# Optimization experiments

Hardware: AMD Instinct MI355X
Metric: run time of the kernel (lower is better)

The kernel has to match this reference:

```python
import jax, jax.numpy as jnp
import numpy as np
from jax import lax

W_BCE, W_DICE, W_FT, W_HD = 1.0, 1.0, 1.0, 0.1
TV_ALPHA, TV_BETA, TV_GAMMA = 0.7, 0.3, 0.75
HD_MAX_DIST, HD_BK = 10, 3
SMOOTH, EPS, HD_EPS = 1e-6, 1e-7, 1e-8


def _max_pool(x, k):
    # torch F.max_pool2d pads with -inf implicitly
    pad = k // 2
    return lax.reduce_window(x, -jnp.inf, lax.max, (1, 1, k, k), (1, 1, 1, 1),
                             [(0, 0), (0, 0), (pad, pad), (pad, pad)])


def _min_pool(x, k):
    pad = k // 2
    return lax.reduce_window(x, jnp.inf, lax.min, (1, 1, k, k), (1, 1, 1, 1),
                             [(0, 0), (0, 0), (pad, pad), (pad, pad)])


def _soft_boundary(mask, k):
    dil = _max_pool(mask, k)
    ero = _min_pool(mask, k)  # == -max_pool(-mask)
    return jnp.maximum(dil - ero, 0.0)


def _bce_with_logits(logits, target):
    # numerically stable: max(x,0) - x*t + log1p(exp(-|x|))
    return jnp.mean(jnp.maximum(logits, 0.0) - logits * target +
                    jnp.log1p(jnp.exp(-jnp.abs(logits))))


def _dice_loss(probs, target):
    p = probs.reshape(probs.shape[0], -1)
    t = target.reshape(target.shape[0], -1)
    inter = jnp.sum(p * t, axis=1)
    denom = jnp.sum(p, axis=1) + jnp.sum(t, axis=1)
    dice = (2.0 * inter + SMOOTH) / (denom + SMOOTH + EPS)
    return jnp.mean(1.0 - dice)


def _focal_tversky(probs, target):
    p = probs.reshape(probs.shape[0], -1)
    t = target.reshape(target.shape[0], -1)
    TP = jnp.sum(p * t, axis=1)
    FP = jnp.sum(p * (1.0 - t), axis=1)
    FN = jnp.sum((1.0 - p) * t, axis=1)
    tv = (TP + SMOOTH) / (TP + TV_ALPHA * FP + TV_BETA * FN + SMOOTH + EPS)
    return jnp.mean(jnp.power(1.0 - tv, TV_GAMMA))


def _hausdorff_surrogate(probs, target):
    pred_b = _soft_boundary(probs, HD_BK)
    gt_b = _soft_boundary(target, HD_BK)
    total = jnp.zeros((), probs.dtype)
    weight_sum = 0.0
    for d in range(1, HD_MAX_DIST + 1):
        pred_d = _max_pool(pred_b, 2 * d + 1)
        gt_d = _max_pool(gt_b, 2 * d + 1)
        w = float(d) / float(HD_MAX_DIST)
        total = total + w * (jnp.mean(jnp.abs(pred_d - gt_b)) +
                             jnp.mean(jnp.abs(gt_d - pred_b)))
        weight_sum += w
    return total / (weight_sum + HD_EPS)


def setup_inputs() -> dict:
    key = jax.random.key(0)
    k1, k2 = jax.random.split(key)
    B, C, H, W = 16, 1, 512, 512
    logits = jax.random.normal(k1, (B, C, H, W), dtype=jnp.float32)
    target = jax.random.randint(k2, (B, C, H, W), 0, 2, dtype=jnp.int32)
    return {"logits": logits, "target": target}


def reference(logits, target):
    t = target.astype(jnp.float32)
    bce = _bce_with_logits(logits, t)
    probs = jax.nn.sigmoid(logits)
    d = _dice_loss(probs, t)
    ft = _focal_tversky(probs, t)
    hd = _hausdorff_surrogate(probs, t)
    return W_BCE * bce + W_DICE * d + W_FT * ft + W_HD * hd
```

## Files before the change

kernel.cpp:

```cpp
#include <hip/hip_runtime.h>
#include <math.h>

namespace {

constexpr int B = 16, H = 512, W = 512;
constexpr int HWc = H * W;
constexpr size_t Nc = (size_t)B * HWc;

constexpr int NSTRIP = 13;
constexpr int CENT = 42;
constexpr int NBAND = 16;
constexpr int NWORK = NSTRIP * NBAND * B * 2;
constexpr int NSB = NWORK / 4;
constexpr int NBCE = B * 64;


template <int CTRL>
__device__ __forceinline__ float dpp_shift1(float v) {
  int i = __float_as_int(v);
  int r = __builtin_amdgcn_update_dpp(i, i, CTRL, 0xF, 0xF, false);
  return __int_as_float(r);
}
template <int CTRL>
__device__ __forceinline__ unsigned dpp_shift1u(unsigned v) {
  return (unsigned)__builtin_amdgcn_update_dpp((int)v, (int)v, CTRL, 0xF, 0xF,
                                               false);
}

__device__ __forceinline__ float hmax3(float v) {
  return fmaxf(fmaxf(dpp_shift1<0x138>(v), v), dpp_shift1<0x130>(v));
}
__device__ __forceinline__ void hminmax3(float v, float& mx, float& mn) {
  float s1 = dpp_shift1<0x138>(v);
  float s2 = dpp_shift1<0x130>(v);
  mx = fmaxf(fmaxf(s1, v), s2);
  mn = fminf(fminf(s1, v), s2);
}

__device__ __forceinline__ unsigned long long or3_lanes(unsigned long long v) {
  unsigned lo = (unsigned)v, hi = (unsigned)(v >> 32);
  unsigned rlo = dpp_shift1u<0x138>(lo) | lo | dpp_shift1u<0x130>(lo);
  unsigned rhi = dpp_shift1u<0x138>(hi) | hi | dpp_shift1u<0x130>(hi);
  return ((unsigned long long)rhi << 32) | rlo;
}
__device__ __forceinline__ unsigned long long and3_lanes(unsigned long long v) {
  unsigned lo = (unsigned)v, hi = (unsigned)(v >> 32);
  unsigned rlo = dpp_shift1u<0x138>(lo) & lo & dpp_shift1u<0x130>(lo);
  unsigned rhi = dpp_shift1u<0x138>(hi) & hi & dpp_shift1u<0x130>(hi);
  return ((unsigned long long)rhi << 32) | rlo;
}

__device__ __forceinline__ float wave_sum(float v) {
#pragma unroll
  for (int off = 32; off > 0; off >>= 1) v += __shfl_down(v, off);
  return v;
}

__device__ __forceinline__ float block_reduce_256(float v, float* sm, int tid) {
#pragma unroll
  for (int off = 32; off > 0; off >>= 1) v += __shfl_down(v, off);
  int lane = tid & 63, wid = tid >> 6;
  if (lane == 0) sm[wid] = v;
  __syncthreads();
  float r = 0.f;
  if (tid == 0) r = sm[0] + sm[1] + sm[2] + sm[3];
  __syncthreads();
  return r;
}

template <int CH>
__device__ __forceinline__ float load_src(const float* __restrict__ Lg,
                                          const int* __restrict__ Tg, int gy,
                                          int colc) {
  gy = min(max(gy, 0), H - 1);
  if constexpr (CH == 0) {
    float x = Lg[gy * W + colc];
    float e = __expf(-x);
    return __builtin_amdgcn_rcpf(1.f + e);
  } else {
    return (float)Tg[gy * W + colc];
  }
}

template <int D>
__device__ __forceinline__ void dilate_steps(float (&a)[52],
                                             const float (&o)[32],
                                             float (&accv)[4]) {
  if constexpr (D <= 10) {
    float hp = hmax3(a[D - 1]);
    float hc = hmax3(a[D]);
#pragma unroll
    for (int r = D; r <= 51 - D; ++r) {
      float hn = hmax3(a[r + 1]);
      float nv = fmaxf(fmaxf(hp, hc), hn);
      hp = hc;
      hc = hn;
      a[r] = nv;
    }
    constexpr float wd = 0.1f * (float)D;
#pragma unroll
    for (int k = 0; k < 32; ++k) accv[k & 3] += wd * fabsf(a[10 + k] - o[k]);
    dilate_steps<D + 1>(a, o, accv);
  }
}

__device__ __forceinline__ void fused_body0(const float* __restrict__ Lg,
                                            const int* __restrict__ Tg,
                                            int lane, int strip, int band,
                                            int bz,
                                            float* __restrict__ chain_p) {
  int col = strip * CENT - 11 + lane;
  int colc = min(max(col, 0), W - 1);
  int y0 = band * 32;

  float o[32];
  {
    float v0 = load_src<1>(Lg, Tg, y0 - 1, colc);
    float v1 = load_src<1>(Lg, Tg, y0, colc);
    float hx0, hn0, hx1, hn1;
    hminmax3(v0, hx0, hn0);
    hminmax3(v1, hx1, hn1);
#pragma unroll
    for (int k = 0; k < 32; ++k) {
      float v2 = load_src<1>(Lg, Tg, y0 + 1 + k, colc);
      float hx2, hn2;
      hminmax3(v2, hx2, hn2);
      o[k] = fmaxf(fmaxf(hx0, hx1), hx2) - fminf(fminf(hn0, hn1), hn2);
      hx0 = hx1;
      hx1 = hx2;
      hn0 = hn1;
      hn1 = hn2;
    }
  }

  float a[52];
  {
    float v0 = load_src<0>(Lg, Tg, y0 - 11, colc);
    float v1 = load_src<0>(Lg, Tg, y0 - 10, colc);
    float hx0, hn0, hx1, hn1;
    hminmax3(v0, hx0, hn0);
    hminmax3(v1, hx1, hn1);
#pragma unroll
    for (int r = 0; r < 52; ++r) {
      float v2 = load_src<0>(Lg, Tg, y0 - 9 + r, colc);
      float hx2, hn2;
      hminmax3(v2, hx2, hn2);
      a[r] = fmaxf(fmaxf(hx0, hx1), hx2) - fminf(fminf(hn0, hn1), hn2);
      hx0 = hx1;
      hx1 = hx2;
      hn0 = hn1;
      hn1 = hn2;
    }
  }

  float accv[4] = {0.f, 0.f, 0.f, 0.f};
  dilate_steps<1>(a, o, accv);
  float acc = (accv[0] + accv[1]) + (accv[2] + accv[3]);

  bool valid = (lane >= 11 && lane <= 52 && col < W);
  acc = valid ? acc : 0.f;
  acc = wave_sum(acc);
  if (lane == 0) chain_p[(bz * NBAND + band) * NSTRIP + strip] = acc;
}

__device__ __forceinline__ void fused_body1(const float* __restrict__ Lg,
                                            const int* __restrict__ Tg,
                                            int lane, int strip, int band,
                                            int bz,
                                            float* __restrict__ chain_p) {
  int col = strip * CENT - 11 + lane;
  int colc = min(max(col, 0), W - 1);
  int y0 = band * 32;

  float o[32];
  {
    float v0 = load_src<0>(Lg, Tg, y0 - 1, colc);
    float v1 = load_src<0>(Lg, Tg, y0, colc);
    float hx0, hn0, hx1, hn1;
    hminmax3(v0, hx0, hn0);
    hminmax3(v1, hx1, hn1);
#pragma unroll
    for (int k = 0; k < 32; ++k) {
      float v2 = load_src<0>(Lg, Tg, y0 + 1 + k, colc);
      float hx2, hn2;
      hminmax3(v2, hx2, hn2);
      o[k] = fmaxf(fmaxf(hx0, hx1), hx2) - fminf(fminf(hn0, hn1), hn2);
      hx0 = hx1;
      hx1 = hx2;
      hn0 = hn1;
      hn1 = hn2;
    }
  }

  unsigned long long tb = 0ull;
#pragma unroll
  for (int j = 0; j < 54; ++j) {
    int gy = min(max(y0 - 11 + j, 0), H - 1);
    tb |= (unsigned long long)(unsigned)Tg[gy * W + colc] << j;
  }

  unsigned long long vd = tb | (tb << 1) | (tb >> 1);
  unsigned long long ve = tb & (tb << 1) & (tb >> 1);
  unsigned long long ab = (or3_lanes(vd) & ~and3_lanes(ve)) >> 1;

  float accv[4] = {0.f, 0.f, 0.f, 0.f};
#pragma unroll
  for (int d = 1; d <= 10; ++d) {
    unsigned long long s = ab | (ab << 1) | (ab >> 1);
    ab = or3_lanes(s);
    const float wd = 0.1f * (float)d;
    unsigned lo = (unsigned)ab, hi = (unsigned)(ab >> 32);
#pragma unroll
    for (int k = 0; k < 32; ++k) {
      unsigned bit =
          (k < 22) ? ((lo >> (10 + k)) & 1u) : ((hi >> (k - 22)) & 1u);
      accv[k & 3] += wd * fabsf((float)bit - o[k]);
    }
  }
  float acc = (accv[0] + accv[1]) + (accv[2] + accv[3]);

  bool valid = (lane >= 11 && lane <= 52 && col < W);
  acc = valid ? acc : 0.f;
  acc = wave_sum(acc);
  if (lane == 0) chain_p[(bz * NBAND + band) * NSTRIP + strip] = acc;
}

__device__ __forceinline__ void bce_body(const float* __restrict__ logits,
                                         const int* __restrict__ target,
                                         int blk, float* __restrict__ bceA,
                                         float* __restrict__ spA,
                                         float* __restrict__ stA,
                                         float* __restrict__ sptA, float* sm) {
  int img = blk >> 6, seg = blk & 63;
  const float4* L4 =
      (const float4*)(logits + (size_t)img * HWc + (size_t)seg * 4096);
  const int4* T4 =
      (const int4*)(target + (size_t)img * HWc + (size_t)seg * 4096);
  int tid = threadIdx.x;
  float s_bce = 0.f, s_p = 0.f, s_t = 0.f, s_pt = 0.f;
#pragma unroll
  for (int it = 0; it < 4; ++it) {
    float4 x4 = L4[it * 256 + tid];
    int4 t4 = T4[it * 256 + tid];
    float xs[4] = {x4.x, x4.y, x4.z, x4.w};
    int ts[4] = {t4.x, t4.y, t4.z, t4.w};
#pragma unroll
    for (int j = 0; j < 4; ++j) {
      float x = xs[j];
      float tf = (float)ts[j];
      float e = __expf(-x);
      float p = __builtin_amdgcn_rcpf(1.f + e);
      s_p += p;
      s_t += tf;
      s_pt += p * tf;
      s_bce += x * (1.f - tf) + __logf(1.f + e);
    }
  }
  float r;
  r = block_reduce_256(s_bce, sm, tid);
  if (tid == 0) bceA[blk] = r;
  r = block_reduce_256(s_p, sm, tid);
  if (tid == 0) spA[blk] = r;
  r = block_reduce_256(s_t, sm, tid);
  if (tid == 0) stA[blk] = r;
  r = block_reduce_256(s_pt, sm, tid);
  if (tid == 0) sptA[blk] = r;
}

__global__ void __launch_bounds__(256, 4) fused_kernel(
    const float* __restrict__ logits, const int* __restrict__ target,
    float* __restrict__ bceA, float* __restrict__ spA,
    float* __restrict__ stA, float* __restrict__ sptA,
    float* __restrict__ chain_p) {
  __shared__ float smr[4];
  int tid = threadIdx.x;
  if (blockIdx.x < NBCE) {
    bce_body(logits, target, blockIdx.x, bceA, spA, stA, sptA, smr);
    return;
  }
  int lane = tid & 63;
  int wv = __builtin_amdgcn_readfirstlane(tid >> 6);
  int widx = (blockIdx.x - NBCE) * 4 + wv;
  int strip = widx % NSTRIP;
  int rest = widx / NSTRIP;
  int band = rest & 15;
  int bz = rest >> 4;
  int img = bz & 15, chain = bz >> 4;
  const float* Lg = logits + (size_t)img * HWc;
  const int* Tg = target + (size_t)img * HWc;
  if (chain == 0)
    fused_body0(Lg, Tg, lane, strip, band, bz, chain_p);
  else
    fused_body1(Lg, Tg, lane, strip, band, bz, chain_p);
}

__global__ void finalize_kernel(const float* __restrict__ bceA,
                                const float* __restrict__ spA,
                                const float* __restrict__ stA,
                                const float* __restrict__ sptA,
                                const float* __restrict__ chain_p,
                                float* __restrict__ out) {
  __shared__ float smr[4];
  __shared__ float smImg[16][3];
  __shared__ double smd[16][2];
  int tid = threadIdx.x;

  float s = 0.f;
  {
    const float4* b4 = (const float4*)bceA;
    for (int i = tid; i < NBCE / 4; i += 256) {
      float4 v = b4[i];
      s += (v.x + v.y) + (v.z + v.w);
    }
  }
  float bce_sum = block_reduce_256(s, smr, tid);

  s = 0.f;
  {
    const float4* c4 = (const float4*)chain_p;
    for (int i = tid; i < NWORK / 4; i += 256) {
      float4 v = c4[i];
      s += (v.x + v.y) + (v.z + v.w);
    }
  }
  float hd_sum = block_reduce_256(s, smr, tid);

  {
    int img = tid >> 4, part = tid & 15;
    float sp = 0.f, st = 0.f, spt = 0.f;
    for (int j = part; j < 64; j += 16) {
      int idx = img * 64 + j;
      sp += spA[idx];
      st += stA[idx];
      spt += sptA[idx];
    }
#pragma unroll
    for (int off = 8; off > 0; off >>= 1) {
      sp += __shfl_down(sp, off, 16);
      st += __shfl_down(st, off, 16);
      spt += __shfl_down(spt, off, 16);
    }
    if (part == 0) {
      smImg[img][0] = sp;
      smImg[img][1] = st;
      smImg[img][2] = spt;
    }
  }
  __syncthreads();
  if (tid < 16) {
    double sp = smImg[tid][0], st = smImg[tid][1], spt = smImg[tid][2];
    double dice = (2.0 * spt + 1e-6) / (sp + st + 1e-6 + 1e-7);
    double tv = (spt + 1e-6) /
                (spt + 0.7 * (sp - spt) + 0.3 * (st - spt) + 1e-6 + 1e-7);
    smd[tid][0] = 1.0 - dice;
    smd[tid][1] = pow(1.0 - tv, 0.75);
  }
  __syncthreads();
  if (tid == 0) {
    double dice_l = 0.0, ft_l = 0.0;
    for (int i = 0; i < 16; ++i) {
      dice_l += smd[i][0];
      ft_l += smd[i][1];
    }
    dice_l /= 16.0;
    ft_l /= 16.0;
    const double Nd = (double)Nc;
    double bce = (double)bce_sum / Nd;
    double hd = ((double)hd_sum / Nd) / (5.5 + 1e-8);
    out[0] = (float)(bce + dice_l + ft_l + 0.1 * hd);
  }
}

}

extern "C" void kernel_launch(void* const* d_in, const int* in_sizes, int n_in,
                              void* d_out, int out_size, void* d_ws,
                              size_t ws_size, hipStream_t stream) {
  const float* logits = (const float*)d_in[0];
  const int* target = (const int*)d_in[1];
  float* out = (float*)d_out;

  float* part = (float*)d_ws;
  float* bceA = part;
  float* spA = part + NBCE;
  float* stA = part + 2 * NBCE;
  float* sptA = part + 3 * NBCE;
  float* chain_p = part + 4 * NBCE;

  fused_kernel<<<dim3(NBCE + NSB), dim3(256), 0, stream>>>(
      logits, target, bceA, spA, stA, sptA, chain_p);
  finalize_kernel<<<1, 256, 0, stream>>>(bceA, spA, stA, sptA, chain_p, out);
}
```

Before: 119.4 us.

## Merge both Hausdorff chains into one wave sharing boundary computations

Instead of launching separate waves for the pred-dilation and gt-dilation chains, each wave now computes the prediction soft boundary and the target bit boundary once. It then runs both dilation chains, deriving the 32 central rows of each boundary from the shared 52-row and bit arrays. This removes the duplicated sigmoid loads and boundary computations and halves the wave count. The cost is more serial work and higher register pressure per wave, so occupancy and latency hiding may drop.

```diff
diff --git a/kernel.cpp b/kernel.cpp
--- a/kernel.cpp
+++ b/kernel.cpp
@@ -11,7 +11,8 @@
 constexpr int CENT = 42;
 constexpr int NBAND = 16;
 constexpr int NWORK = NSTRIP * NBAND * B * 2;
-constexpr int NSB = NWORK / 4;
+constexpr int NMERGED = NSTRIP * NBAND * B;
+constexpr int NSB = NMERGED / 4;
 constexpr int NBCE = B * 64;
 
 
@@ -68,18 +69,12 @@
   return r;
 }
 
-template <int CH>
-__device__ __forceinline__ float load_src(const float* __restrict__ Lg,
-                                          const int* __restrict__ Tg, int gy,
-                                          int colc) {
+__device__ __forceinline__ float sigmoid_at(const float* __restrict__ Lg,
+                                            int gy, int colc) {
   gy = min(max(gy, 0), H - 1);
-  if constexpr (CH == 0) {
-    float x = Lg[gy * W + colc];
-    float e = __expf(-x);
-    return __builtin_amdgcn_rcpf(1.f + e);
-  } else {
-    return (float)Tg[gy * W + colc];
-  }
+  float x = Lg[gy * W + colc];
+  float e = __expf(-x);
+  return __builtin_amdgcn_rcpf(1.f + e);
 }
 
 template <int D>
@@ -104,45 +99,25 @@
   }
 }
 
-__device__ __forceinline__ void fused_body0(const float* __restrict__ Lg,
-                                            const int* __restrict__ Tg,
-                                            int lane, int strip, int band,
-                                            int bz,
-                                            float* __restrict__ chain_p) {
+__device__ __forceinline__ void fused_body(const float* __restrict__ Lg,
+                                           const int* __restrict__ Tg,
+                                           int lane, int strip, int band,
+                                           int img,
+                                           float* __restrict__ chain_p) {
   int col = strip * CENT - 11 + lane;
   int colc = min(max(col, 0), W - 1);
   int y0 = band * 32;
 
-  float o[32];
-  {
-    float v0 = load_src<1>(Lg, Tg, y0 - 1, colc);
-    float v1 = load_src<1>(Lg, Tg, y0, colc);
+  float a[52];
+  {
+    float v0 = sigmoid_at(Lg, y0 - 11, colc);
+    float v1 = sigmoid_at(Lg, y0 - 10, colc);
     float hx0, hn0, hx1, hn1;
     hminmax3(v0, hx0, hn0);
     hminmax3(v1, hx1, hn1);
 #pragma unroll
-    for (int k = 0; k < 32; ++k) {
-      float v2 = load_src<1>(Lg, Tg, y0 + 1 + k, colc);
-      float hx2, hn2;
-      hminmax3(v2, hx2, hn2);
-      o[k] = fmaxf(fmaxf(hx0, hx1), hx2) - fminf(fminf(hn0, hn1), hn2);
-      hx0 = hx1;
-      hx1 = hx2;
-      hn0 = hn1;
-      hn1 = hn2;
-    }
-  }
-
-  float a[52];
-  {
-    float v0 = load_src<0>(Lg, Tg, y0 - 11, colc);
-    float v1 = load_src<0>(Lg, Tg, y0 - 10, colc);
-    float hx0, hn0, hx1, hn1;
-    hminmax3(v0, hx0, hn0);
-    hminmax3(v1, hx1, hn1);
-#pragma unroll
     for (int r = 0; r < 52; ++r) {
-      float v2 = load_src<0>(Lg, Tg, y0 - 9 + r, colc);
+      float v2 = sigmoid_at(Lg, y0 - 9 + r, colc);
       float hx2, hn2;
       hminmax3(v2, hx2, hn2);
       a[r] = fmaxf(fmaxf(hx0, hx1), hx2) - fminf(fminf(hn0, hn1), hn2);
@@ -153,76 +128,62 @@
     }
   }
 
-  float accv[4] = {0.f, 0.f, 0.f, 0.f};
-  dilate_steps<1>(a, o, accv);
-  float acc = (accv[0] + accv[1]) + (accv[2] + accv[3]);
-
-  bool valid = (lane >= 11 && lane <= 52 && col < W);
-  acc = valid ? acc : 0.f;
-  acc = wave_sum(acc);
-  if (lane == 0) chain_p[(bz * NBAND + band) * NSTRIP + strip] = acc;
-}
-
-__device__ __forceinline__ void fused_body1(const float* __restrict__ Lg,
-                                            const int* __restrict__ Tg,
-                                            int lane, int strip, int band,
-                                            int bz,
-                                            float* __restrict__ chain_p) {
-  int col = strip * CENT - 11 + lane;
-  int colc = min(max(col, 0), W - 1);
-  int y0 = band * 32;
-
-  float o[32];
-  {
-    float v0 = load_src<0>(Lg, Tg, y0 - 1, colc);
-    float v1 = load_src<0>(Lg, Tg, y0, colc);
-    float hx0, hn0, hx1, hn1;
-    hminmax3(v0, hx0, hn0);
-    hminmax3(v1, hx1, hn1);
-#pragma unroll
-    for (int k = 0; k < 32; ++k) {
-      float v2 = load_src<0>(Lg, Tg, y0 + 1 + k, colc);
-      float hx2, hn2;
-      hminmax3(v2, hx2, hn2);
-      o[k] = fmaxf(fmaxf(hx0, hx1), hx2) - fminf(fminf(hn0, hn1), hn2);
-      hx0 = hx1;
-      hx1 = hx2;
-      hn0 = hn1;
-      hn1 = hn2;
-    }
-  }
-
-  unsigned long long tb = 0ull;
-#pragma unroll
-  for (int j = 0; j < 54; ++j) {
-    int gy = min(max(y0 - 11 + j, 0), H - 1);
-    tb |= (unsigned long long)(unsigned)Tg[gy * W + colc] << j;
-  }
-
-  unsigned long long vd = tb | (tb << 1) | (tb >> 1);
-  unsigned long long ve = tb & (tb << 1) & (tb >> 1);
-  unsigned long long ab = (or3_lanes(vd) & ~and3_lanes(ve)) >> 1;
-
-  float accv[4] = {0.f, 0.f, 0.f, 0.f};
-#pragma unroll
-  for (int d = 1; d <= 10; ++d) {
-    unsigned long long s = ab | (ab << 1) | (ab >> 1);
-    ab = or3_lanes(s);
-    const float wd = 0.1f * (float)d;
-    unsigned lo = (unsigned)ab, hi = (unsigned)(ab >> 32);
+  unsigned long long ab0;
+  {
+    unsigned long long tb = 0ull;
+#pragma unroll
+    for (int j = 0; j < 54; ++j) {
+      int gy = min(max(y0 - 11 + j, 0), H - 1);
+      tb |= (unsigned long long)(unsigned)Tg[gy * W + colc] << j;
+    }
+    unsigned long long vd = tb | (tb << 1) | (tb >> 1);
+    unsigned long long ve = tb & (tb << 1) & (tb >> 1);
+    ab0 = (or3_lanes(vd) & ~and3_lanes(ve)) >> 1;
+  }
+
+  float accv1[4] = {0.f, 0.f, 0.f, 0.f};
+  {
+    unsigned long long ab = ab0;
+#pragma unroll
+    for (int d = 1; d <= 10; ++d) {
+      unsigned long long s = ab | (ab << 1) | (ab >> 1);
+      ab = or3_lanes(s);
+      const float wd = 0.1f * (float)d;
+      unsigned lo = (unsigned)ab, hi = (unsigned)(ab >> 32);
+#pragma unroll
+      for (int k = 0; k < 32; ++k) {
+        unsigned bit =
+            (k < 22) ? ((lo >> (10 + k)) & 1u) : ((hi >> (k - 22)) & 1u);
+        accv1[k & 3] += wd * fabsf((float)bit - a[10 + k]);
+      }
+    }
+  }
+  float acc1 = (accv1[0] + accv1[1]) + (accv1[2] + accv1[3]);
+
+  float o0[32];
+  {
+    unsigned lo = (unsigned)ab0, hi = (unsigned)(ab0 >> 32);
 #pragma unroll
     for (int k = 0; k < 32; ++k) {
       unsigned bit =
           (k < 22) ? ((lo >> (10 + k)) & 1u) : ((hi >> (k - 22)) & 1u);
-      accv[k & 3] += wd * fabsf((float)bit - o[k]);
-    }
-  }
-  float acc = (accv[0] + accv[1]) + (accv[2] + accv[3]);
+      o0[k] = (float)bit;
+    }
+  }
+
+  float accv0[4] = {0.f, 0.f, 0.f, 0.f};
+  dilate_steps<1>(a, o0, accv0);
+  float acc0 = (accv0[0] + accv0[1]) + (accv0[2] + accv0[3]);
 
   bool valid = (lane >= 11 && lane <= 52 && col < W);
-  acc = valid ? acc : 0.f;
-  acc = wave_sum(acc);
-  if (lane == 0) chain_p[(bz * NBAND + band) * NSTRIP + strip] = acc;
+  acc0 = valid ? acc0 : 0.f;
+  acc1 = valid ? acc1 : 0.f;
+  acc0 = wave_sum(acc0);
+  acc1 = wave_sum(acc1);
+  if (lane == 0) {
+    chain_p[(img * NBAND + band) * NSTRIP + strip] = acc0;
+    chain_p[((16 + img) * NBAND + band) * NSTRIP + strip] = acc1;
+  }
 }
 
 __device__ __forceinline__ void bce_body(const float* __restrict__ logits,
@@ -284,14 +245,10 @@
   int strip = widx % NSTRIP;
   int rest = widx / NSTRIP;
   int band = rest & 15;
-  int bz = rest >> 4;
-  int img = bz & 15, chain = bz >> 4;
+  int img = rest >> 4;
   const float* Lg = logits + (size_t)img * HWc;
   const int* Tg = target + (size_t)img * HWc;
-  if (chain == 0)
-    fused_body0(Lg, Tg, lane, strip, band, bz, chain_p);
-  else
-    fused_body1(Lg, Tg, lane, strip, band, bz, chain_p);
+  fused_body(Lg, Tg, lane, strip, band, img, chain_p);
 }
 
 __global__ void finalize_kernel(const float* __restrict__ bceA,
```

New measurement: 130.7 us. 9.5% more time.
